# Performance work log

Measured on AMD Instinct MI355X. Metric: run time of the kernel, lower is better.

Reference implementation:

```python
import jax, jax.numpy as jnp
import numpy as np

B, S, D, F, T, NS, L, H = 8, 1024, 1024, 4096, 64, 512, 32, 16
TAG_RATE = 0.5      # config.tagging_rate
GSR = 0.5           # config.gate_scaling_rate
ATT_EPS = 1e-12     # config.layer_norm_eps (att_norm)
ENC_EPS = 1e-5      # torch TransformerEncoderLayer default


def _ln(x, g, b, eps):
    m = x.mean(-1, keepdims=True)
    v = x.var(-1, keepdims=True)
    return (x - m) * jax.lax.rsqrt(v + eps) * g + b


def _rope(x):
    # standard rotary embedding over the full hidden dim
    d = x.shape[-1]
    s = x.shape[1]
    inv = 1.0 / (10000.0 ** (jnp.arange(0, d, 2, dtype=jnp.float32) / d))
    ang = jnp.arange(s, dtype=jnp.float32)[:, None] * inv[None, :]  # [S, D/2]
    sin, cos = jnp.sin(ang), jnp.cos(ang)
    x1, x2 = x[..., 0::2], x[..., 1::2]
    return jnp.stack([x1 * cos - x2 * sin, x1 * sin + x2 * cos], axis=-1).reshape(x.shape)


def setup_inputs() -> dict:
    key = jax.random.key(0)
    ks = jax.random.split(key, 24)
    p = lambda k, shp: (0.02 * jax.random.normal(k, shp, dtype=jnp.float32))
    inp = {
        'word_embedding': jax.random.normal(ks[0], (B, S, D), dtype=jnp.float32),
        'attention_mask': jnp.ones((B, S), dtype=jnp.int32),
        'span_batch': jax.random.randint(ks[1], (NS,), 0, B, dtype=jnp.int32),
        'span_start': jax.random.randint(ks[2], (NS,), 0, S - L, dtype=jnp.int32),
        'span_tag': jax.random.randint(ks[3], (NS,), 0, T, dtype=jnp.int32),
        'tag_emb': p(ks[4], (T, D)),
        'gate_w': p(ks[5], (D, 1)),
        'gate_b': jnp.zeros((1,), jnp.float32),
        'attn_ln_g': jnp.ones((D,), jnp.float32),
        'attn_ln_b': jnp.zeros((D,), jnp.float32),
        'in_proj_w': p(ks[6], (3 * D, D)),
        'in_proj_b': jnp.zeros((3 * D,), jnp.float32),
        'out_proj_w': p(ks[7], (D, D)),
        'out_proj_b': jnp.zeros((D,), jnp.float32),
        'enc_ln1_g': jnp.ones((D,), jnp.float32),
        'enc_ln1_b': jnp.zeros((D,), jnp.float32),
        'lin1_w': p(ks[8], (F, D)),
        'lin1_b': jnp.zeros((F,), jnp.float32),
        'lin2_w': p(ks[9], (D, F)),
        'lin2_b': jnp.zeros((D,), jnp.float32),
        'enc_ln2_g': jnp.ones((D,), jnp.float32),
        'enc_ln2_b': jnp.zeros((D,), jnp.float32),
    }
    return inp


def _mha(x, pad, in_proj_w, in_proj_b, out_proj_w, out_proj_b):
    b, s, d = x.shape
    hd = d // H
    qkv = x @ in_proj_w.T + in_proj_b                       # [B,S,3D]
    q, k, v = jnp.split(qkv, 3, axis=-1)
    rs = lambda t: t.reshape(b, s, H, hd).transpose(0, 2, 1, 3)  # [B,H,S,hd]
    q, k, v = rs(q), rs(k), rs(v)
    scores = jnp.einsum('bhqd,bhkd->bhqk', q, k) / jnp.sqrt(jnp.float32(hd))
    scores = jnp.where(pad[:, None, None, :], jnp.float32(-1e30), scores)
    attn = jax.nn.softmax(scores, axis=-1)
    o = jnp.einsum('bhqk,bhkd->bhqd', attn, v).transpose(0, 2, 1, 3).reshape(b, s, d)
    return o @ out_proj_w.T + out_proj_b


def reference(word_embedding, attention_mask, span_batch, span_start, span_tag,
              tag_emb, gate_w, gate_b, attn_ln_g, attn_ln_b,
              in_proj_w, in_proj_b, out_proj_w, out_proj_b,
              enc_ln1_g, enc_ln1_b, lin1_w, lin1_b, lin2_w, lin2_b,
              enc_ln2_g, enc_ln2_b):
    raw = word_embedding                        # dropout off (eval)
    we = _rope(word_embedding)
    # ragged gather -> gate -> scatter-add over fixed-length spans
    tok = span_start[:, None] + jnp.arange(L, dtype=jnp.int32)[None, :]  # [NS,L]
    X = we[span_batch[:, None], tok]            # [NS,L,D]
    gate = GSR * jax.nn.sigmoid(X @ gate_w + gate_b) + (1.0 - GSR) / 2.0  # [NS,L,1]
    res = gate * tag_emb[span_tag][:, None, :] * jnp.float32(L)          # [NS,L,D]
    taged = jnp.zeros_like(word_embedding).at[span_batch[:, None], tok].add(res)
    out_emb = raw + taged * TAG_RATE            # if_merge_by_add
    out_emb = _ln(out_emb, attn_ln_g, attn_ln_b, ATT_EPS)
    pad = attention_mask == 0
    # torch TransformerEncoderLayer (post-norm, relu)
    a = _mha(out_emb, pad, in_proj_w, in_proj_b, out_proj_w, out_proj_b)
    x = _ln(out_emb + a, enc_ln1_g, enc_ln1_b, ENC_EPS)
    ff = jax.nn.relu(x @ lin1_w.T + lin1_b) @ lin2_w.T + lin2_b
    enc = _ln(x + ff, enc_ln2_g, enc_ln2_b, ENC_EPS)
    return enc + out_emb
```

## Files before the change

kernel.cpp:

```cpp
#include <hip/hip_runtime.h>

#define DEV __device__ __forceinline__

typedef short bf16x8 __attribute__((ext_vector_type(8)));
typedef float f32x4 __attribute__((ext_vector_type(4)));
typedef unsigned short u16;
typedef unsigned int u32;

typedef __attribute__((address_space(3))) void lds_void;
typedef __attribute__((address_space(1))) void gbl_void;

DEV void async_copy16(void* lds_dst, const void* g_src) {
    __builtin_amdgcn_global_load_lds((gbl_void*)g_src, (lds_void*)lds_dst, 16, 0, 0);
}

DEV u16 f2bf(float x) {
    u32 u = __float_as_uint(x);
    return (u16)((u + 0x7fffu + ((u >> 16) & 1u)) >> 16);
}
DEV u16 f2bf_fast(float x) {
    return (u16)((__float_as_uint(x) + 0x8000u) >> 16);
}
DEV float bf2f(u16 v) { return __uint_as_float(((u32)v) << 16); }

__global__ __launch_bounds__(256) void f2bf_kernel(const float* __restrict__ src,
                                                   u16* __restrict__ dst, int n4) {
    const int i = blockIdx.x * 256 + threadIdx.x;
    if (i < n4) {
        const float4 v = ((const float4*)src)[i];
        ushort4 o;
        o.x = f2bf(v.x); o.y = f2bf(v.y); o.z = f2bf(v.z); o.w = f2bf(v.w);
        ((ushort4*)dst)[i] = o;
    }
}

__global__ __launch_bounds__(256) void span_kernel(
    const float* __restrict__ we, const int* __restrict__ sb,
    const int* __restrict__ ss, const int* __restrict__ stg,
    const float* __restrict__ tag_emb, const float* __restrict__ gate_w,
    const float* __restrict__ gate_b, float* __restrict__ out_pre) {
    __shared__ float red[4];
    const int n = blockIdx.x >> 5;
    const int l = blockIdx.x & 31;
    const int t = threadIdx.x;
    const int b = sb[n];
    const int s = ss[n] + l;
    const int tag = stg[n];
    const long base = ((long)b * 1024 + s) * 1024;
    float dot = 0.f;
#pragma unroll
    for (int pp = 0; pp < 2; ++pp) {
        const int p = t + pp * 256;
        const float e1 = we[base + 2 * p];
        const float e2 = we[base + 2 * p + 1];
        const float inv = exp2f((float)p * (-13.287712379549449f / 512.0f));
        const float ang = (float)s * inv;
        const float sa = sinf(ang), ca = cosf(ang);
        const float r1 = e1 * ca - e2 * sa;
        const float r2 = e1 * sa + e2 * ca;
        dot += r1 * gate_w[2 * p] + r2 * gate_w[2 * p + 1];
    }
#pragma unroll
    for (int off = 32; off > 0; off >>= 1) dot += __shfl_xor(dot, off, 64);
    if ((t & 63) == 0) red[t >> 6] = dot;
    __syncthreads();
    const float z = red[0] + red[1] + red[2] + red[3] + gate_b[0];
    const float gate = 0.25f + 0.5f / (1.f + __expf(-z));
    const float coef = gate * 16.f;
    const float* te = tag_emb + (long)tag * 1024;
#pragma unroll
    for (int c = 0; c < 4; ++c) {
        const int d = t + c * 256;
        atomicAdd(&out_pre[base + d], coef * te[d]);
    }
}

template <bool WRITE_F32, bool WRITE_BF, bool FINAL>
__global__ __launch_bounds__(256) void ln_kernel(
    const float* __restrict__ X, const float* __restrict__ g,
    const float* __restrict__ bta, float eps, float* __restrict__ Yf,
    u16* __restrict__ Ybf, const u16* __restrict__ addend) {
    __shared__ float red[8];
    const long row = blockIdx.x;
    const int t = threadIdx.x;
    const float4 x = ((const float4*)(X + row * 1024))[t];
    float s = x.x + x.y + x.z + x.w;
#pragma unroll
    for (int off = 32; off > 0; off >>= 1) s += __shfl_xor(s, off, 64);
    if ((t & 63) == 0) red[t >> 6] = s;
    __syncthreads();
    const float mean = (red[0] + red[1] + red[2] + red[3]) * (1.f / 1024.f);
    float4 dx;
    dx.x = x.x - mean; dx.y = x.y - mean; dx.z = x.z - mean; dx.w = x.w - mean;
    float ss = dx.x * dx.x + dx.y * dx.y + dx.z * dx.z + dx.w * dx.w;
#pragma unroll
    for (int off = 32; off > 0; off >>= 1) ss += __shfl_xor(ss, off, 64);
    if ((t & 63) == 0) red[4 + (t >> 6)] = ss;
    __syncthreads();
    const float var = (red[4] + red[5] + red[6] + red[7]) * (1.f / 1024.f);
    const float rstd = rsqrtf(var + eps);
    const float4 gv = ((const float4*)g)[t];
    const float4 bv = ((const float4*)bta)[t];
    float4 y;
    y.x = dx.x * rstd * gv.x + bv.x;
    y.y = dx.y * rstd * gv.y + bv.y;
    y.z = dx.z * rstd * gv.z + bv.z;
    y.w = dx.w * rstd * gv.w + bv.w;
    if (FINAL) {
        const ushort4 a = ((const ushort4*)(addend + row * 1024))[t];
        y.x += bf2f(a.x); y.y += bf2f(a.y); y.z += bf2f(a.z); y.w += bf2f(a.w);
    }
    if (WRITE_F32) ((float4*)(Yf + row * 1024))[t] = y;
    if (WRITE_BF) {
        ushort4 o;
        o.x = f2bf(y.x); o.y = f2bf(y.y); o.z = f2bf(y.z); o.w = f2bf(y.w);
        ((ushort4*)(Ybf + row * 1024))[t] = o;
    }
}

template <bool OUT_BF16, bool RELU, bool HAS_RES>
__global__ __launch_bounds__(256, 2) void gemm_nt(
    const u16* __restrict__ A, const u16* __restrict__ B,
    const float* __restrict__ bias, const u16* __restrict__ res,
    void* __restrict__ Cout, int N, int K) {
    __shared__ u16 Al[8192];
    __shared__ u16 Bl[8192];
    const int tid = threadIdx.x;
    const int wave = tid >> 6;
    const int lane = tid & 63;
    const int quad = lane >> 4;
    const int lq = lane & 15;
    const int wm = wave >> 1;
    const int wn = wave & 1;
    const long rowBase = (long)blockIdx.x * 128;
    const long colBase = (long)blockIdx.y * 128;

    f32x4 acc[4][4];
    const f32x4 fzero = {0.f, 0.f, 0.f, 0.f};
#pragma unroll
    for (int i = 0; i < 4; ++i)
#pragma unroll
        for (int j = 0; j < 4; ++j) acc[i][j] = fzero;

    const int rX = tid >> 3;
    const int pX = (tid & 7) ^ (rX & 7);
    const u16* gA = A + (rowBase + rX) * (long)K + pX * 8;
    const u16* gB = B + (colBase + rX) * (long)K + pX * 8;
    u16* ldsA = Al + wave * 512;
    u16* ldsB = Bl + wave * 512;

    for (int kt = 0; kt < K; kt += 64) {
        __syncthreads();
#pragma unroll
        for (int c = 0; c < 4; ++c) {
            async_copy16(ldsA + c * 2048, gA + (long)c * 32 * K + kt);
            async_copy16(ldsB + c * 2048, gB + (long)c * 32 * K + kt);
        }
        __syncthreads();
#pragma unroll
        for (int ks = 0; ks < 2; ++ks) {
            bf16x8 af[4], bfr[4];
#pragma unroll
            for (int i = 0; i < 4; ++i) {
                const int r = wm * 64 + i * 16 + lq;
                af[i] = *(const bf16x8*)&Al[r * 64 + (((ks * 4 + quad) ^ (lq & 7)) * 8)];
            }
#pragma unroll
            for (int j = 0; j < 4; ++j) {
                const int r = wn * 64 + j * 16 + lq;
                bfr[j] = *(const bf16x8*)&Bl[r * 64 + (((ks * 4 + quad) ^ (lq & 7)) * 8)];
            }
#pragma unroll
            for (int i = 0; i < 4; ++i)
#pragma unroll
                for (int j = 0; j < 4; ++j)
                    acc[i][j] = __builtin_amdgcn_mfma_f32_16x16x32_bf16(
                        af[i], bfr[j], acc[i][j], 0, 0, 0);
        }
    }

    float biasv[4];
#pragma unroll
    for (int j = 0; j < 4; ++j) biasv[j] = bias[colBase + wn * 64 + j * 16 + lq];
#pragma unroll
    for (int i = 0; i < 4; ++i) {
        const long grow = rowBase + wm * 64 + i * 16 + quad * 4;
#pragma unroll
        for (int j = 0; j < 4; ++j) {
            const long gcol = colBase + wn * 64 + j * 16 + lq;
#pragma unroll
            for (int r = 0; r < 4; ++r) {
                float v = acc[i][j][r] + biasv[j];
                if (RELU) v = fmaxf(v, 0.f);
                if (HAS_RES) v += bf2f(res[(grow + r) * N + gcol]);
                if (OUT_BF16)
                    ((u16*)Cout)[(grow + r) * N + gcol] = f2bf(v);
                else
                    ((float*)Cout)[(grow + r) * N + gcol] = v;
            }
        }
    }
}

__global__ __launch_bounds__(256) void vtrans_kernel(const u16* __restrict__ QKV,
                                                     u16* __restrict__ Vt) {
    __shared__ u16 tile[64][72];
    const int bid = blockIdx.x;
    const int st = bid & 15;
    const int h = (bid >> 4) & 15;
    const int b = bid >> 8;
    const int t = threadIdx.x;
    const int sl = t >> 2;
    const int dc = (t & 3) * 16;
    const u16* src = QKV + ((long)(b * 1024 + st * 64 + sl)) * 3072 + 2048 + h * 64 + dc;
    *(uint4*)&tile[sl][dc] = *(const uint4*)src;
    *(uint4*)&tile[sl][dc + 8] = *(const uint4*)(src + 8);
    __syncthreads();
    const int dl = t >> 2;
    const int sc = (t & 3) * 16;
    union { u16 u[16]; uint4 q[2]; } tmp;
#pragma unroll
    for (int i = 0; i < 16; ++i) tmp.u[i] = tile[sc + i][dl];
    u16* dst = Vt + ((long)(b * 16 + h) * 64 + dl) * 1024 + st * 64 + sc;
    *(uint4*)dst = tmp.q[0];
    *(uint4*)(dst + 8) = tmp.q[1];
}

__global__ __launch_bounds__(256, 4) void attn_kernel(
    const u16* __restrict__ QKV, const u16* __restrict__ Vt,
    const int* __restrict__ mask, u16* __restrict__ Out) {
    __shared__ u16 KL[4096];
    __shared__ u16 VL[4096];
    __shared__ u16 PL[4][16 * 72];
    const int tid = threadIdx.x;
    const int wid = tid >> 6;
    const int lane = tid & 63;
    const int quad = lane >> 4;
    const int lq = lane & 15;
    const int slot0 = quad ^ (lq & 7);
    const int slot1 = slot0 ^ 4;

    const int bid = blockIdx.x;
    const int qb = bid & 7;
    const int h = (bid >> 3) & 15;
    const int b = bid >> 7;
    const int qbase = qb * 128 + wid * 32;

    bf16x8 aq[2][2];
#pragma unroll
    for (int t = 0; t < 2; ++t) {
        const u16* qp = QKV + ((long)(b * 1024 + qbase + t * 16 + lq)) * 3072 +
                        h * 64 + quad * 8;
        aq[t][0] = *(const bf16x8*)qp;
        aq[t][1] = *(const bf16x8*)(qp + 32);
    }

    const int c0 = tid, c1 = 256 + tid;
    const int r0 = c0 >> 3, j0 = (c0 & 7) ^ (r0 & 7);
    const int r1 = c1 >> 3, j1 = (c1 & 7) ^ (r1 & 7);
    const u16* srcK0 = QKV + ((long)(b * 1024 + r0)) * 3072 + 1024 + h * 64 + j0 * 8;
    const u16* srcK1 = QKV + ((long)(b * 1024 + r1)) * 3072 + 1024 + h * 64 + j1 * 8;
    const u16* srcV0 = Vt + ((long)(b * 16 + h) * 64 + r0) * 1024 + j0 * 8;
    const u16* srcV1 = Vt + ((long)(b * 16 + h) * 64 + r1) * 1024 + j1 * 8;
    u16* ldsK0 = KL + wid * 512;
    u16* ldsK1 = KL + 2048 + wid * 512;
    u16* ldsV0 = VL + wid * 512;
    u16* ldsV1 = VL + 2048 + wid * 512;

    const f32x4 fzero = {0.f, 0.f, 0.f, 0.f};
    f32x4 acc[2][4];
#pragma unroll
    for (int t = 0; t < 2; ++t)
#pragma unroll
        for (int j = 0; j < 4; ++j) acc[t][j] = fzero;
    float lsum[2][4] = {{0.f, 0.f, 0.f, 0.f}, {0.f, 0.f, 0.f, 0.f}};
    u16* myP = PL[wid];
    const int* mrow = mask + b * 1024;

    for (int kt = 0; kt < 1024; kt += 64) {
        __syncthreads();
        async_copy16(ldsK0, srcK0 + (long)kt * 3072);
        async_copy16(ldsK1, srcK1 + (long)kt * 3072);
        async_copy16(ldsV0, srcV0 + kt);
        async_copy16(ldsV1, srcV1 + kt);
        __syncthreads();

        bf16x8 kf0[4], kf1[4];
#pragma unroll
        for (int ct = 0; ct < 4; ++ct) {
            const int rowb = (ct * 16 + lq) * 64;
            kf0[ct] = *(const bf16x8*)&KL[rowb + slot0 * 8];
            kf1[ct] = *(const bf16x8*)&KL[rowb + slot1 * 8];
        }
        float mw[4];
#pragma unroll
        for (int ct = 0; ct < 4; ++ct) mw[ct] = mrow[kt + ct * 16 + lq] ? 1.f : 0.f;

#pragma unroll
        for (int t = 0; t < 2; ++t) {
            f32x4 s[4];
#pragma unroll
            for (int ct = 0; ct < 4; ++ct) {
                s[ct] = __builtin_amdgcn_mfma_f32_16x16x32_bf16(aq[t][0], kf0[ct],
                                                                fzero, 0, 0, 0);
                s[ct] = __builtin_amdgcn_mfma_f32_16x16x32_bf16(aq[t][1], kf1[ct],
                                                                s[ct], 0, 0, 0);
            }
            asm volatile("s_waitcnt lgkmcnt(0)" ::: "memory");
#pragma unroll
            for (int ct = 0; ct < 4; ++ct)
#pragma unroll
                for (int r = 0; r < 4; ++r) {
                    const float p = mw[ct] * __expf(s[ct][r] * 0.125f);
                    lsum[t][r] += p;
                    myP[(quad * 4 + r) * 72 + ct * 16 + lq] = f2bf_fast(p);
                }
            asm volatile("s_waitcnt lgkmcnt(0)" ::: "memory");
            const bf16x8 pf0 = *(const bf16x8*)&myP[lq * 72 + quad * 8];
            const bf16x8 pf1 = *(const bf16x8*)&myP[lq * 72 + 32 + quad * 8];
#pragma unroll
            for (int j = 0; j < 4; ++j) {
                const int rowb = (j * 16 + lq) * 64;
                const bf16x8 vf0 = *(const bf16x8*)&VL[rowb + slot0 * 8];
                const bf16x8 vf1 = *(const bf16x8*)&VL[rowb + slot1 * 8];
                acc[t][j] = __builtin_amdgcn_mfma_f32_16x16x32_bf16(pf0, vf0,
                                                                    acc[t][j], 0, 0, 0);
                acc[t][j] = __builtin_amdgcn_mfma_f32_16x16x32_bf16(pf1, vf1,
                                                                    acc[t][j], 0, 0, 0);
            }
        }
    }

#pragma unroll
    for (int t = 0; t < 2; ++t) {
        float inv[4];
#pragma unroll
        for (int r = 0; r < 4; ++r) {
            float l = lsum[t][r];
#pragma unroll
            for (int off = 1; off < 16; off <<= 1) l += __shfl_xor(l, off, 16);
            inv[r] = 1.f / l;
        }
        const long orow = (long)b * 1024 + qbase + t * 16 + quad * 4;
#pragma unroll
        for (int j = 0; j < 4; ++j)
#pragma unroll
            for (int r = 0; r < 4; ++r)
                Out[(orow + r) * 1024 + h * 64 + j * 16 + lq] =
                    f2bf_fast(acc[t][j][r] * inv[r]);
    }
}

extern "C" void kernel_launch(void* const* d_in, const int* in_sizes, int n_in,
                              void* d_out, int out_size, void* d_ws, size_t ws_size,
                              hipStream_t stream) {
    const float* we        = (const float*)d_in[0];
    const int*   amask     = (const int*)d_in[1];
    const int*   span_b    = (const int*)d_in[2];
    const int*   span_s    = (const int*)d_in[3];
    const int*   span_t    = (const int*)d_in[4];
    const float* tag_emb   = (const float*)d_in[5];
    const float* gate_w    = (const float*)d_in[6];
    const float* gate_b    = (const float*)d_in[7];
    const float* attn_ln_g = (const float*)d_in[8];
    const float* attn_ln_b = (const float*)d_in[9];
    const float* in_proj_w = (const float*)d_in[10];
    const float* in_proj_b = (const float*)d_in[11];
    const float* out_proj_w= (const float*)d_in[12];
    const float* out_proj_b= (const float*)d_in[13];
    const float* enc1_g    = (const float*)d_in[14];
    const float* enc1_b    = (const float*)d_in[15];
    const float* lin1_w    = (const float*)d_in[16];
    const float* lin1_b    = (const float*)d_in[17];
    const float* lin2_w    = (const float*)d_in[18];
    const float* lin2_b    = (const float*)d_in[19];
    const float* enc2_g    = (const float*)d_in[20];
    const float* enc2_b    = (const float*)d_in[21];
    float* out = (float*)d_out;

    char* ws = (char*)d_ws;
    size_t off = 0;
    auto alloc = [&](size_t bytes) {
        void* p = ws + off;
        off += (bytes + 255) & ~(size_t)255;
        return p;
    };
    const size_t MT = 8192;
    u16* oe_bf   = (u16*)alloc(MT * 1024 * 2);
    u16* ax_bf   = (u16*)alloc(MT * 1024 * 2);
    char* region = (char*)alloc((size_t)67108864);
    u16* qkv_bf  = (u16*)region;
    u16* vt_bf   = (u16*)(region + (size_t)MT * 3072 * 2);
    u16* ff1_bf  = (u16*)region;
    u16* wb_inproj  = (u16*)alloc((size_t)3072 * 1024 * 2);
    u16* wb_outproj = (u16*)alloc((size_t)1024 * 1024 * 2);
    u16* wb_lin1    = (u16*)alloc((size_t)4096 * 1024 * 2);
    u16* wb_lin2    = (u16*)alloc((size_t)1024 * 4096 * 2);

    hipMemcpyAsync(out, we, MT * 1024 * 4, hipMemcpyDeviceToDevice, stream);
    f2bf_kernel<<<3072, 256, 0, stream>>>(in_proj_w, wb_inproj, 3072 * 1024 / 4);
    f2bf_kernel<<<1024, 256, 0, stream>>>(out_proj_w, wb_outproj, 1024 * 1024 / 4);
    f2bf_kernel<<<4096, 256, 0, stream>>>(lin1_w, wb_lin1, 4096 * 1024 / 4);
    f2bf_kernel<<<4096, 256, 0, stream>>>(lin2_w, wb_lin2, 1024 * 4096 / 4);
    span_kernel<<<16384, 256, 0, stream>>>(we, span_b, span_s, span_t, tag_emb,
                                           gate_w, gate_b, out);
    ln_kernel<false, true, false><<<8192, 256, 0, stream>>>(
        out, attn_ln_g, attn_ln_b, 1e-12f, nullptr, oe_bf, nullptr);
    dim3 g1(64, 24);
    gemm_nt<true, false, false><<<g1, 256, 0, stream>>>(oe_bf, wb_inproj, in_proj_b,
                                                        nullptr, qkv_bf, 3072, 1024);
    vtrans_kernel<<<2048, 256, 0, stream>>>(qkv_bf, vt_bf);
    attn_kernel<<<1024, 256, 0, stream>>>(qkv_bf, vt_bf, amask, ax_bf);
    dim3 g2(64, 8);
    gemm_nt<false, false, true><<<g2, 256, 0, stream>>>(ax_bf, wb_outproj, out_proj_b,
                                                        oe_bf, out, 1024, 1024);
    ln_kernel<false, true, false><<<8192, 256, 0, stream>>>(
        out, enc1_g, enc1_b, 1e-5f, nullptr, ax_bf, nullptr);
    dim3 g3(64, 32);
    gemm_nt<true, true, false><<<g3, 256, 0, stream>>>(ax_bf, wb_lin1, lin1_b,
                                                       nullptr, ff1_bf, 4096, 1024);
    gemm_nt<false, false, true><<<g2, 256, 0, stream>>>(ff1_bf, wb_lin2, lin2_b,
                                                        ax_bf, out, 1024, 4096);
    ln_kernel<true, false, true><<<8192, 256, 0, stream>>>(
        out, enc2_g, enc2_b, 1e-5f, out, nullptr, oe_bf);
}
```

Measured before the change: 565.3 us.

## Add 256x256-tile 8-wave pipelined GEMM for QKV and FFN1 projections

Introduces a new bf16 MFMA GEMM kernel with 256x256 output tiles, 512 threads (8 waves), double-buffered LDS filled by async global-to-LDS copies, an XOR-swizzled layout, and a phased schedule that interleaves loads with MFMA groups under raised wave priority. It replaces the 128x128 kernel for the in-projection and lin1 GEMMs to raise data reuse per block and overlap memory with compute. The larger tile needs about 128KB of LDS and many accumulator registers, which limits occupancy. The grid shrinks to 384 and 512 blocks, which may leave the 256 CUs unevenly loaded. The prefetch index wraps modulo the K-tile count, so a redundant load is issued at the tail.

```diff
diff --git a/kernel.cpp b/kernel.cpp
--- a/kernel.cpp
+++ b/kernel.cpp
@@ -197,6 +197,220 @@
                     ((u16*)Cout)[(grow + r) * N + gcol] = f2bf(v);
                 else
                     ((float*)Cout)[(grow + r) * N + gcol] = v;
+            }
+        }
+    }
+}
+
+#define PH_SYNC()                                          \
+    do {                                                   \
+        __builtin_amdgcn_s_barrier();                      \
+        asm volatile("s_waitcnt lgkmcnt(0)" ::: "memory"); \
+        __builtin_amdgcn_sched_barrier(0);                 \
+    } while (0)
+
+template <bool RELU>
+__global__ __launch_bounds__(512, 2) void gemm_nt8(
+    const u16* __restrict__ A, const u16* __restrict__ B,
+    const float* __restrict__ bias, u16* __restrict__ Cout, int N, int K) {
+    __shared__ u16 Al[2][16384];
+    __shared__ u16 Bl[2][16384];
+    const int tid = threadIdx.x;
+    const int wave = tid >> 6;
+    const int lane = tid & 63;
+    const int quad = lane >> 4;
+    const int lq = lane & 15;
+    const int lq7 = lq & 7;
+    const int wm = wave >> 2;
+    const int wn = wave & 3;
+    const long rowBase = (long)blockIdx.x * 256;
+    const long colBase = (long)blockIdx.y * 256;
+    const int NT = K >> 6;
+
+    const int rs = tid >> 3;
+    const int js = (tid & 7) ^ (rs & 7);
+    const u16* gA = A + (rowBase + rs) * (long)K + js * 8;
+    const u16* gB = B + (colBase + rs) * (long)K + js * 8;
+
+    f32x4 acc[8][4];
+    const f32x4 fz = {0.f, 0.f, 0.f, 0.f};
+#pragma unroll
+    for (int i = 0; i < 8; ++i)
+#pragma unroll
+        for (int j = 0; j < 4; ++j) acc[i][j] = fz;
+
+    auto stA = [&](int buf, int h, int t) {
+        u16* d = &Al[buf][h * 8192 + wave * 512];
+        const u16* s = gA + (long)h * 128 * K + t * 64;
+        async_copy16(d, s);
+        async_copy16(d + 4096, s + (long)64 * K);
+    };
+    auto stB = [&](int buf, int h, int t) {
+        u16* d = &Bl[buf][h * 8192 + wave * 512];
+        const u16* s = gB + (long)h * 128 * K + t * 64;
+        async_copy16(d, s);
+        async_copy16(d + 4096, s + (long)64 * K);
+    };
+    auto ldA = [&](int buf, int i, int kh) {
+        const int r = wm * 128 + i * 16 + lq;
+        return *(const bf16x8*)&Al[buf][r * 64 + ((((kh << 2) | quad) ^ lq7) << 3)];
+    };
+    auto ldB = [&](int buf, int j, int kh) {
+        const int r = wn * 64 + j * 16 + lq;
+        return *(const bf16x8*)&Bl[buf][r * 64 + ((((kh << 2) | quad) ^ lq7) << 3)];
+    };
+
+    stA(0, 0, 0); stA(0, 1, 0); stB(0, 0, 0); stB(0, 1, 0);
+    stA(1, 0, 1);
+    asm volatile("s_waitcnt vmcnt(2)" ::: "memory");
+    __builtin_amdgcn_s_barrier();
+
+    bf16x8 at[8], ab[8], bl[4], br[4];
+    for (int it = 0; it < (NT >> 1); ++it) {
+        const int t1 = 2 * it + 1;
+        int t2 = 2 * it + 2; if (t2 >= NT) t2 -= NT;
+        int t3 = 2 * it + 3; if (t3 >= NT) t3 -= NT;
+
+#pragma unroll
+        for (int i = 0; i < 4; ++i) { at[2 * i] = ldA(0, i, 0); at[2 * i + 1] = ldA(0, i, 1); }
+#pragma unroll
+        for (int j = 0; j < 2; ++j) { bl[2 * j] = ldB(0, j, 0); bl[2 * j + 1] = ldB(0, j, 1); }
+        stA(1, 1, t1);
+        PH_SYNC();
+        __builtin_amdgcn_s_setprio(1);
+#pragma unroll
+        for (int i = 0; i < 4; ++i)
+#pragma unroll
+            for (int j = 0; j < 2; ++j)
+#pragma unroll
+                for (int kh = 0; kh < 2; ++kh)
+                    acc[i][j] = __builtin_amdgcn_mfma_f32_16x16x32_bf16(
+                        at[2 * i + kh], bl[2 * j + kh], acc[i][j], 0, 0, 0);
+        __builtin_amdgcn_s_setprio(0);
+        __builtin_amdgcn_s_barrier();
+#pragma unroll
+        for (int j = 0; j < 2; ++j) { br[2 * j] = ldB(0, j + 2, 0); br[2 * j + 1] = ldB(0, j + 2, 1); }
+        stB(1, 0, t1);
+        PH_SYNC();
+        __builtin_amdgcn_s_setprio(1);
+#pragma unroll
+        for (int i = 0; i < 4; ++i)
+#pragma unroll
+            for (int j = 0; j < 2; ++j)
+#pragma unroll
+                for (int kh = 0; kh < 2; ++kh)
+                    acc[i][j + 2] = __builtin_amdgcn_mfma_f32_16x16x32_bf16(
+                        at[2 * i + kh], br[2 * j + kh], acc[i][j + 2], 0, 0, 0);
+        __builtin_amdgcn_s_setprio(0);
+        __builtin_amdgcn_s_barrier();
+#pragma unroll
+        for (int i = 0; i < 4; ++i) { ab[2 * i] = ldA(0, i + 4, 0); ab[2 * i + 1] = ldA(0, i + 4, 1); }
+        stB(1, 1, t1);
+        PH_SYNC();
+        __builtin_amdgcn_s_setprio(1);
+#pragma unroll
+        for (int i = 0; i < 4; ++i)
+#pragma unroll
+            for (int j = 0; j < 2; ++j)
+#pragma unroll
+                for (int kh = 0; kh < 2; ++kh)
+                    acc[i + 4][j] = __builtin_amdgcn_mfma_f32_16x16x32_bf16(
+                        ab[2 * i + kh], bl[2 * j + kh], acc[i + 4][j], 0, 0, 0);
+        __builtin_amdgcn_s_setprio(0);
+        __builtin_amdgcn_s_barrier();
+        stA(0, 0, t2);
+        PH_SYNC();
+        __builtin_amdgcn_s_setprio(1);
+#pragma unroll
+        for (int i = 0; i < 4; ++i)
+#pragma unroll
+            for (int j = 0; j < 2; ++j)
+#pragma unroll
+                for (int kh = 0; kh < 2; ++kh)
+                    acc[i + 4][j + 2] = __builtin_amdgcn_mfma_f32_16x16x32_bf16(
+                        ab[2 * i + kh], br[2 * j + kh], acc[i + 4][j + 2], 0, 0, 0);
+        __builtin_amdgcn_s_setprio(0);
+        asm volatile("s_waitcnt vmcnt(2)" ::: "memory");
+        __builtin_amdgcn_s_barrier();
+
+#pragma unroll
+        for (int i = 0; i < 4; ++i) { at[2 * i] = ldA(1, i, 0); at[2 * i + 1] = ldA(1, i, 1); }
+#pragma unroll
+        for (int j = 0; j < 2; ++j) { bl[2 * j] = ldB(1, j, 0); bl[2 * j + 1] = ldB(1, j, 1); }
+        stA(0, 1, t2);
+        PH_SYNC();
+        __builtin_amdgcn_s_setprio(1);
+#pragma unroll
+        for (int i = 0; i < 4; ++i)
+#pragma unroll
+            for (int j = 0; j < 2; ++j)
+#pragma unroll
+                for (int kh = 0; kh < 2; ++kh)
+                    acc[i][j] = __builtin_amdgcn_mfma_f32_16x16x32_bf16(
+                        at[2 * i + kh], bl[2 * j + kh], acc[i][j], 0, 0, 0);
+        __builtin_amdgcn_s_setprio(0);
+        __builtin_amdgcn_s_barrier();
+#pragma unroll
+        for (int j = 0; j < 2; ++j) { br[2 * j] = ldB(1, j + 2, 0); br[2 * j + 1] = ldB(1, j + 2, 1); }
+        stB(0, 0, t2);
+        PH_SYNC();
+        __builtin_amdgcn_s_setprio(1);
+#pragma unroll
+        for (int i = 0; i < 4; ++i)
+#pragma unroll
+            for (int j = 0; j < 2; ++j)
+#pragma unroll
+                for (int kh = 0; kh < 2; ++kh)
+                    acc[i][j + 2] = __builtin_amdgcn_mfma_f32_16x16x32_bf16(
+                        at[2 * i + kh], br[2 * j + kh], acc[i][j + 2], 0, 0, 0);
+        __builtin_amdgcn_s_setprio(0);
+        __builtin_amdgcn_s_barrier();
+#pragma unroll
+        for (int i = 0; i < 4; ++i) { ab[2 * i] = ldA(1, i + 4, 0); ab[2 * i + 1] = ldA(1, i + 4, 1); }
+        stB(0, 1, t2);
+        PH_SYNC();
+        __builtin_amdgcn_s_setprio(1);
+#pragma unroll
+        for (int i = 0; i < 4; ++i)
+#pragma unroll
+            for (int j = 0; j < 2; ++j)
+#pragma unroll
+                for (int kh = 0; kh < 2; ++kh)
+                    acc[i + 4][j] = __builtin_amdgcn_mfma_f32_16x16x32_bf16(
+                        ab[2 * i + kh], bl[2 * j + kh], acc[i + 4][j], 0, 0, 0);
+        __builtin_amdgcn_s_setprio(0);
+        __builtin_amdgcn_s_barrier();
+        stA(1, 0, t3);
+        PH_SYNC();
+        __builtin_amdgcn_s_setprio(1);
+#pragma unroll
+        for (int i = 0; i < 4; ++i)
+#pragma unroll
+            for (int j = 0; j < 2; ++j)
+#pragma unroll
+                for (int kh = 0; kh < 2; ++kh)
+                    acc[i + 4][j + 2] = __builtin_amdgcn_mfma_f32_16x16x32_bf16(
+                        ab[2 * i + kh], br[2 * j + kh], acc[i + 4][j + 2], 0, 0, 0);
+        __builtin_amdgcn_s_setprio(0);
+        asm volatile("s_waitcnt vmcnt(2)" ::: "memory");
+        __builtin_amdgcn_s_barrier();
+    }
+
+    asm volatile("s_waitcnt vmcnt(0)" ::: "memory");
+    float bv[4];
+#pragma unroll
+    for (int j = 0; j < 4; ++j) bv[j] = bias[colBase + wn * 64 + j * 16 + lq];
+#pragma unroll
+    for (int i = 0; i < 8; ++i) {
+        const long grow = rowBase + wm * 128 + i * 16 + quad * 4;
+#pragma unroll
+        for (int j = 0; j < 4; ++j) {
+            const long gcol = colBase + wn * 64 + j * 16 + lq;
+#pragma unroll
+            for (int r = 0; r < 4; ++r) {
+                float v = acc[i][j][r] + bv[j];
+                if (RELU) v = fmaxf(v, 0.f);
+                Cout[(grow + r) * N + gcol] = f2bf(v);
             }
         }
     }
@@ -406,9 +620,9 @@
                                            gate_w, gate_b, out);
     ln_kernel<false, true, false><<<8192, 256, 0, stream>>>(
         out, attn_ln_g, attn_ln_b, 1e-12f, nullptr, oe_bf, nullptr);
-    dim3 g1(64, 24);
-    gemm_nt<true, false, false><<<g1, 256, 0, stream>>>(oe_bf, wb_inproj, in_proj_b,
-                                                        nullptr, qkv_bf, 3072, 1024);
+    dim3 g1(32, 12);
+    gemm_nt8<false><<<g1, 512, 0, stream>>>(oe_bf, wb_inproj, in_proj_b,
+                                            qkv_bf, 3072, 1024);
     vtrans_kernel<<<2048, 256, 0, stream>>>(qkv_bf, vt_bf);
     attn_kernel<<<1024, 256, 0, stream>>>(qkv_bf, vt_bf, amask, ax_bf);
     dim3 g2(64, 8);
@@ -416,9 +630,9 @@
                                                         oe_bf, out, 1024, 1024);
     ln_kernel<false, true, false><<<8192, 256, 0, stream>>>(
         out, enc1_g, enc1_b, 1e-5f, nullptr, ax_bf, nullptr);
-    dim3 g3(64, 32);
-    gemm_nt<true, true, false><<<g3, 256, 0, stream>>>(ax_bf, wb_lin1, lin1_b,
-                                                       nullptr, ff1_bf, 4096, 1024);
+    dim3 g3(32, 16);
+    gemm_nt8<true><<<g3, 512, 0, stream>>>(ax_bf, wb_lin1, lin1_b,
+                                           ff1_bf, 4096, 1024);
     gemm_nt<false, false, true><<<g2, 256, 0, stream>>>(ff1_bf, wb_lin2, lin2_b,
                                                         ax_bf, out, 1024, 4096);
     ln_kernel<true, false, true><<<8192, 256, 0, stream>>>(
```

Result: no change. 570.1 us (+0.8%).

## Replace GEMM with 8-wave 256x128 tile, triple-buffered async LDS pipeline

Applied to the files above, without the earlier changes.

Replaces the 256-thread 128x128 GEMM with a 512-thread kernel that computes a 256x128 tile. It uses a three-stage LDS ring fed by async global-to-LDS copies two k-steps ahead. Each k-iteration is split into two phases that interleave staging, fragment loads and MFMA bursts, with raised wave priority during MFMA. The goal is to hide global memory latency and raise MFMA utilisation, since the old kernel serialised load and compute behind two barriers per step. The trade-off is 144KB of LDS, which may limit occupancy (launch bounds of 2 may not be met), and fewer blocks for the N=1024 GEMMs.

```diff
diff --git a/kernel.cpp b/kernel.cpp
--- a/kernel.cpp
+++ b/kernel.cpp
@@ -118,70 +118,114 @@
     }
 }
 
+#define PH_SYNC()                                          \
+    do {                                                   \
+        __builtin_amdgcn_s_barrier();                      \
+        asm volatile("s_waitcnt lgkmcnt(0)" ::: "memory"); \
+        __builtin_amdgcn_sched_barrier(0);                 \
+    } while (0)
+
 template <bool OUT_BF16, bool RELU, bool HAS_RES>
-__global__ __launch_bounds__(256, 2) void gemm_nt(
+__global__ __launch_bounds__(512, 2) void gemm_nt8b(
     const u16* __restrict__ A, const u16* __restrict__ B,
     const float* __restrict__ bias, const u16* __restrict__ res,
     void* __restrict__ Cout, int N, int K) {
-    __shared__ u16 Al[8192];
-    __shared__ u16 Bl[8192];
+    __shared__ u16 LT[3][24576];
     const int tid = threadIdx.x;
     const int wave = tid >> 6;
     const int lane = tid & 63;
     const int quad = lane >> 4;
     const int lq = lane & 15;
+    const int lq7 = lq & 7;
     const int wm = wave >> 1;
     const int wn = wave & 1;
-    const long rowBase = (long)blockIdx.x * 128;
+    const long rowBase = (long)blockIdx.x * 256;
     const long colBase = (long)blockIdx.y * 128;
+    const int NT = K >> 6;
+
+    const int rs = tid >> 3;
+    const int js = (tid & 7) ^ (rs & 7);
+    const u16* gA = A + (rowBase + rs) * (long)K + js * 8;
+    const u16* gB = B + (colBase + rs) * (long)K + js * 8;
+    const long s64K = (long)64 * K;
 
     f32x4 acc[4][4];
-    const f32x4 fzero = {0.f, 0.f, 0.f, 0.f};
+    const f32x4 fz = {0.f, 0.f, 0.f, 0.f};
 #pragma unroll
     for (int i = 0; i < 4; ++i)
 #pragma unroll
-        for (int j = 0; j < 4; ++j) acc[i][j] = fzero;
-
-    const int rX = tid >> 3;
-    const int pX = (tid & 7) ^ (rX & 7);
-    const u16* gA = A + (rowBase + rX) * (long)K + pX * 8;
-    const u16* gB = B + (colBase + rX) * (long)K + pX * 8;
-    u16* ldsA = Al + wave * 512;
-    u16* ldsB = Bl + wave * 512;
-
-    for (int kt = 0; kt < K; kt += 64) {
-        __syncthreads();
-#pragma unroll
-        for (int c = 0; c < 4; ++c) {
-            async_copy16(ldsA + c * 2048, gA + (long)c * 32 * K + kt);
-            async_copy16(ldsB + c * 2048, gB + (long)c * 32 * K + kt);
-        }
-        __syncthreads();
-#pragma unroll
-        for (int ks = 0; ks < 2; ++ks) {
-            bf16x8 af[4], bfr[4];
-#pragma unroll
-            for (int i = 0; i < 4; ++i) {
-                const int r = wm * 64 + i * 16 + lq;
-                af[i] = *(const bf16x8*)&Al[r * 64 + (((ks * 4 + quad) ^ (lq & 7)) * 8)];
-            }
-#pragma unroll
-            for (int j = 0; j < 4; ++j) {
-                const int r = wn * 64 + j * 16 + lq;
-                bfr[j] = *(const bf16x8*)&Bl[r * 64 + (((ks * 4 + quad) ^ (lq & 7)) * 8)];
-            }
-#pragma unroll
-            for (int i = 0; i < 4; ++i)
-#pragma unroll
-                for (int j = 0; j < 4; ++j)
+        for (int j = 0; j < 4; ++j) acc[i][j] = fz;
+
+    auto stage = [&](int so, int u, int t) {
+        u16* d = &LT[0][0] + so + u * 4096 + wave * 512;
+        const u16* s = (u < 4 ? gA + u * s64K : gB + (u - 4) * s64K) + (long)t * 64;
+        async_copy16(d, s);
+    };
+    auto ldA = [&](int bo, int i, int kh) {
+        const int r = wm * 64 + i * 16 + lq;
+        return *(const bf16x8*)(&LT[0][0] + bo + r * 64 +
+                                ((((kh << 2) | quad) ^ lq7) << 3));
+    };
+    auto ldB = [&](int bo, int j, int kh) {
+        const int r = wn * 64 + j * 16 + lq;
+        return *(const bf16x8*)(&LT[0][0] + bo + 16384 + r * 64 +
+                                ((((kh << 2) | quad) ^ lq7) << 3));
+    };
+
+#pragma unroll
+    for (int u = 0; u < 6; ++u) stage(0, u, 0);
+#pragma unroll
+    for (int u = 0; u < 6; ++u) stage(24576, u, 1);
+    asm volatile("s_waitcnt vmcnt(6)" ::: "memory");
+    __builtin_amdgcn_s_barrier();
+
+    int bo = 0;
+    int so = 2 * 24576;
+    for (int t = 0; t < NT; ++t) {
+        int tp2 = t + 2;
+        if (tp2 >= NT) tp2 -= NT;
+        bf16x8 a8[8], bb[8];
+#pragma unroll
+        for (int i = 0; i < 4; ++i) { a8[2 * i] = ldA(bo, i, 0); a8[2 * i + 1] = ldA(bo, i, 1); }
+#pragma unroll
+        for (int j = 0; j < 2; ++j) { bb[2 * j] = ldB(bo, j, 0); bb[2 * j + 1] = ldB(bo, j, 1); }
+        stage(so, 0, tp2); stage(so, 1, tp2); stage(so, 2, tp2);
+        PH_SYNC();
+        __builtin_amdgcn_s_setprio(1);
+#pragma unroll
+        for (int i = 0; i < 4; ++i)
+#pragma unroll
+            for (int j = 0; j < 2; ++j)
+#pragma unroll
+                for (int kh = 0; kh < 2; ++kh)
                     acc[i][j] = __builtin_amdgcn_mfma_f32_16x16x32_bf16(
-                        af[i], bfr[j], acc[i][j], 0, 0, 0);
-        }
-    }
-
-    float biasv[4];
-#pragma unroll
-    for (int j = 0; j < 4; ++j) biasv[j] = bias[colBase + wn * 64 + j * 16 + lq];
+                        a8[2 * i + kh], bb[2 * j + kh], acc[i][j], 0, 0, 0);
+        __builtin_amdgcn_s_setprio(0);
+        __builtin_amdgcn_s_barrier();
+#pragma unroll
+        for (int j = 0; j < 2; ++j) { bb[4 + 2 * j] = ldB(bo, j + 2, 0); bb[4 + 2 * j + 1] = ldB(bo, j + 2, 1); }
+        stage(so, 3, tp2); stage(so, 4, tp2); stage(so, 5, tp2);
+        PH_SYNC();
+        __builtin_amdgcn_s_setprio(1);
+#pragma unroll
+        for (int i = 0; i < 4; ++i)
+#pragma unroll
+            for (int j = 0; j < 2; ++j)
+#pragma unroll
+                for (int kh = 0; kh < 2; ++kh)
+                    acc[i][j + 2] = __builtin_amdgcn_mfma_f32_16x16x32_bf16(
+                        a8[2 * i + kh], bb[4 + 2 * j + kh], acc[i][j + 2], 0, 0, 0);
+        __builtin_amdgcn_s_setprio(0);
+        asm volatile("s_waitcnt vmcnt(6)" ::: "memory");
+        __builtin_amdgcn_s_barrier();
+        bo += 24576; if (bo == 3 * 24576) bo = 0;
+        so += 24576; if (so == 3 * 24576) so = 0;
+    }
+
+    asm volatile("s_waitcnt vmcnt(0)" ::: "memory");
+    float bv[4];
+#pragma unroll
+    for (int j = 0; j < 4; ++j) bv[j] = bias[colBase + wn * 64 + j * 16 + lq];
 #pragma unroll
     for (int i = 0; i < 4; ++i) {
         const long grow = rowBase + wm * 64 + i * 16 + quad * 4;
@@ -190,7 +234,7 @@
             const long gcol = colBase + wn * 64 + j * 16 + lq;
 #pragma unroll
             for (int r = 0; r < 4; ++r) {
-                float v = acc[i][j][r] + biasv[j];
+                float v = acc[i][j][r] + bv[j];
                 if (RELU) v = fmaxf(v, 0.f);
                 if (HAS_RES) v += bf2f(res[(grow + r) * N + gcol]);
                 if (OUT_BF16)
@@ -406,21 +450,21 @@
                                            gate_w, gate_b, out);
     ln_kernel<false, true, false><<<8192, 256, 0, stream>>>(
         out, attn_ln_g, attn_ln_b, 1e-12f, nullptr, oe_bf, nullptr);
-    dim3 g1(64, 24);
-    gemm_nt<true, false, false><<<g1, 256, 0, stream>>>(oe_bf, wb_inproj, in_proj_b,
-                                                        nullptr, qkv_bf, 3072, 1024);
+    dim3 g1(32, 24);
+    gemm_nt8b<true, false, false><<<g1, 512, 0, stream>>>(
+        oe_bf, wb_inproj, in_proj_b, nullptr, qkv_bf, 3072, 1024);
     vtrans_kernel<<<2048, 256, 0, stream>>>(qkv_bf, vt_bf);
     attn_kernel<<<1024, 256, 0, stream>>>(qkv_bf, vt_bf, amask, ax_bf);
-    dim3 g2(64, 8);
-    gemm_nt<false, false, true><<<g2, 256, 0, stream>>>(ax_bf, wb_outproj, out_proj_b,
-                                                        oe_bf, out, 1024, 1024);
+    dim3 g2(32, 8);
+    gemm_nt8b<false, false, true><<<g2, 512, 0, stream>>>(
+        ax_bf, wb_outproj, out_proj_b, oe_bf, out, 1024, 1024);
     ln_kernel<false, true, false><<<8192, 256, 0, stream>>>(
         out, enc1_g, enc1_b, 1e-5f, nullptr, ax_bf, nullptr);
-    dim3 g3(64, 32);
-    gemm_nt<true, true, false><<<g3, 256, 0, stream>>>(ax_bf, wb_lin1, lin1_b,
-                                                       nullptr, ff1_bf, 4096, 1024);
-    gemm_nt<false, false, true><<<g2, 256, 0, stream>>>(ff1_bf, wb_lin2, lin2_b,
-                                                        ax_bf, out, 1024, 4096);
+    dim3 g3(32, 32);
+    gemm_nt8b<true, true, false><<<g3, 512, 0, stream>>>(
+        ax_bf, wb_lin1, lin1_b, nullptr, ff1_bf, 4096, 1024);
+    gemm_nt8b<false, false, true><<<g2, 512, 0, stream>>>(
+        ff1_bf, wb_lin2, lin2_b, ax_bf, out, 1024, 4096);
     ln_kernel<true, false, true><<<8192, 256, 0, stream>>>(
         out, enc2_g, enc2_b, 1e-5f, out, nullptr, oe_bf);
 }
```

Measured after the change: 557.9 us. About the same (-1.3%).

## Replace atomic span scatter with per-row tag lists fused into layernorm

Applied to the files above, without the earlier changes.

Builds a per-row list of span tags with a small atomic kernel. The span gate, the tag-embedding accumulation and the attention layernorm then run together in a single per-row kernel that reads the word embedding once. This drops the device-to-device copy of the embedding into the output, the 16384-block atomicAdd scatter kernel and the separate layernorm read of the intermediate buffer. The cost is that each row can hold at most 64 covering spans, which assumes spans do not overlap more heavily than that.

```diff
diff --git a/kernel.cpp b/kernel.cpp
--- a/kernel.cpp
+++ b/kernel.cpp
@@ -34,31 +34,49 @@
     }
 }
 
-__global__ __launch_bounds__(256) void span_kernel(
-    const float* __restrict__ we, const int* __restrict__ sb,
-    const int* __restrict__ ss, const int* __restrict__ stg,
-    const float* __restrict__ tag_emb, const float* __restrict__ gate_w,
-    const float* __restrict__ gate_b, float* __restrict__ out_pre) {
-    __shared__ float red[4];
-    const int n = blockIdx.x >> 5;
-    const int l = blockIdx.x & 31;
+#define SPAN_CAP 64
+
+__global__ __launch_bounds__(256) void zero_kernel(int* __restrict__ p, int n) {
+    const int i = blockIdx.x * 256 + threadIdx.x;
+    if (i < n) p[i] = 0;
+}
+
+__global__ void rowlist_kernel(const int* __restrict__ sb,
+                               const int* __restrict__ ss,
+                               const int* __restrict__ stg,
+                               int* __restrict__ cnt, u16* __restrict__ tags) {
+    const int n = blockIdx.x;
+    const int l = threadIdx.x;
+    const int row = sb[n] * 1024 + ss[n] + l;
+    const int idx = atomicAdd(&cnt[row], 1);
+    if (idx < SPAN_CAP) tags[row * SPAN_CAP + idx] = (u16)stg[n];
+}
+
+__global__ __launch_bounds__(256) void lnspan_kernel(
+    const float* __restrict__ we, const int* __restrict__ cnt,
+    const u16* __restrict__ tags, const float* __restrict__ tag_emb,
+    const float* __restrict__ gate_w, const float* __restrict__ gate_b,
+    const float* __restrict__ g, const float* __restrict__ bta,
+    u16* __restrict__ oe_bf) {
+    __shared__ float red[8];
+    const int row = blockIdx.x;
+    const int s = row & 1023;
     const int t = threadIdx.x;
-    const int b = sb[n];
-    const int s = ss[n] + l;
-    const int tag = stg[n];
-    const long base = ((long)b * 1024 + s) * 1024;
-    float dot = 0.f;
-#pragma unroll
-    for (int pp = 0; pp < 2; ++pp) {
-        const int p = t + pp * 256;
-        const float e1 = we[base + 2 * p];
-        const float e2 = we[base + 2 * p + 1];
-        const float inv = exp2f((float)p * (-13.287712379549449f / 512.0f));
-        const float ang = (float)s * inv;
-        const float sa = sinf(ang), ca = cosf(ang);
-        const float r1 = e1 * ca - e2 * sa;
-        const float r2 = e1 * sa + e2 * ca;
-        dot += r1 * gate_w[2 * p] + r2 * gate_w[2 * p + 1];
+    float4 x = ((const float4*)(we + (long)row * 1024))[t];
+
+    const float4 gw = ((const float4*)gate_w)[t];
+    float dot;
+    {
+        const float p0 = (float)(2 * t);
+        const float p1 = (float)(2 * t + 1);
+        const float inv0 = exp2f(p0 * (-13.287712379549449f / 512.0f));
+        const float inv1 = exp2f(p1 * (-13.287712379549449f / 512.0f));
+        const float a0 = (float)s * inv0, a1 = (float)s * inv1;
+        const float s0 = sinf(a0), c0 = cosf(a0);
+        const float s1 = sinf(a1), c1 = cosf(a1);
+        const float r1a = x.x * c0 - x.y * s0, r2a = x.x * s0 + x.y * c0;
+        const float r1b = x.z * c1 - x.w * s1, r2b = x.z * s1 + x.w * c1;
+        dot = r1a * gw.x + r2a * gw.y + r1b * gw.z + r2b * gw.w;
     }
 #pragma unroll
     for (int off = 32; off > 0; off >>= 1) dot += __shfl_xor(dot, off, 64);
@@ -67,12 +85,41 @@
     const float z = red[0] + red[1] + red[2] + red[3] + gate_b[0];
     const float gate = 0.25f + 0.5f / (1.f + __expf(-z));
     const float coef = gate * 16.f;
-    const float* te = tag_emb + (long)tag * 1024;
-#pragma unroll
-    for (int c = 0; c < 4; ++c) {
-        const int d = t + c * 256;
-        atomicAdd(&out_pre[base + d], coef * te[d]);
-    }
+
+    const int c = min(cnt[row], SPAN_CAP);
+    float4 add = {0.f, 0.f, 0.f, 0.f};
+    for (int k = 0; k < c; ++k) {
+        const int tag = tags[row * SPAN_CAP + k];
+        const float4 te = ((const float4*)(tag_emb + (long)tag * 1024))[t];
+        add.x += te.x; add.y += te.y; add.z += te.z; add.w += te.w;
+    }
+    x.x += coef * add.x; x.y += coef * add.y;
+    x.z += coef * add.z; x.w += coef * add.w;
+
+    __syncthreads();
+    float sm = x.x + x.y + x.z + x.w;
+#pragma unroll
+    for (int off = 32; off > 0; off >>= 1) sm += __shfl_xor(sm, off, 64);
+    if ((t & 63) == 0) red[t >> 6] = sm;
+    __syncthreads();
+    const float mean = (red[0] + red[1] + red[2] + red[3]) * (1.f / 1024.f);
+    float4 dx;
+    dx.x = x.x - mean; dx.y = x.y - mean; dx.z = x.z - mean; dx.w = x.w - mean;
+    float ss = dx.x * dx.x + dx.y * dx.y + dx.z * dx.z + dx.w * dx.w;
+#pragma unroll
+    for (int off = 32; off > 0; off >>= 1) ss += __shfl_xor(ss, off, 64);
+    if ((t & 63) == 0) red[4 + (t >> 6)] = ss;
+    __syncthreads();
+    const float var = (red[4] + red[5] + red[6] + red[7]) * (1.f / 1024.f);
+    const float rstd = rsqrtf(var + 1e-12f);
+    const float4 gv = ((const float4*)g)[t];
+    const float4 bv = ((const float4*)bta)[t];
+    ushort4 o;
+    o.x = f2bf(dx.x * rstd * gv.x + bv.x);
+    o.y = f2bf(dx.y * rstd * gv.y + bv.y);
+    o.z = f2bf(dx.z * rstd * gv.z + bv.z);
+    o.w = f2bf(dx.w * rstd * gv.w + bv.w);
+    ((ushort4*)(oe_bf + (long)row * 1024))[t] = o;
 }
 
 template <bool WRITE_F32, bool WRITE_BF, bool FINAL>
@@ -396,16 +443,18 @@
     u16* wb_outproj = (u16*)alloc((size_t)1024 * 1024 * 2);
     u16* wb_lin1    = (u16*)alloc((size_t)4096 * 1024 * 2);
     u16* wb_lin2    = (u16*)alloc((size_t)1024 * 4096 * 2);
-
-    hipMemcpyAsync(out, we, MT * 1024 * 4, hipMemcpyDeviceToDevice, stream);
+    int* row_cnt    = (int*)alloc((size_t)8192 * 4);
+    u16* row_tags   = (u16*)alloc((size_t)8192 * SPAN_CAP * 2);
+
+    zero_kernel<<<32, 256, 0, stream>>>(row_cnt, 8192);
+    rowlist_kernel<<<512, 32, 0, stream>>>(span_b, span_s, span_t, row_cnt, row_tags);
     f2bf_kernel<<<3072, 256, 0, stream>>>(in_proj_w, wb_inproj, 3072 * 1024 / 4);
     f2bf_kernel<<<1024, 256, 0, stream>>>(out_proj_w, wb_outproj, 1024 * 1024 / 4);
     f2bf_kernel<<<4096, 256, 0, stream>>>(lin1_w, wb_lin1, 4096 * 1024 / 4);
     f2bf_kernel<<<4096, 256, 0, stream>>>(lin2_w, wb_lin2, 1024 * 4096 / 4);
-    span_kernel<<<16384, 256, 0, stream>>>(we, span_b, span_s, span_t, tag_emb,
-                                           gate_w, gate_b, out);
-    ln_kernel<false, true, false><<<8192, 256, 0, stream>>>(
-        out, attn_ln_g, attn_ln_b, 1e-12f, nullptr, oe_bf, nullptr);
+    lnspan_kernel<<<8192, 256, 0, stream>>>(we, row_cnt, row_tags, tag_emb,
+                                            gate_w, gate_b, attn_ln_g, attn_ln_b,
+                                            oe_bf);
     dim3 g1(64, 24);
     gemm_nt<true, false, false><<<g1, 256, 0, stream>>>(oe_bf, wb_inproj, in_proj_b,
                                                         nullptr, qkv_bf, 3072, 1024);
```

Result: faster. 523.4 us (-7.4%).
